# Performance work log

Measured on AMD Instinct MI355X. Metric: run time of the kernel, lower is better.

The kernel has to match this reference:

```python
import jax, jax.numpy as jnp
import numpy as np

HIDDEN = 1024
N_EXPERTS = 8
CAP_FACTOR = 1.1
LN_EPS = 1e-5


def setup_inputs() -> dict:
    key = jax.random.key(0)
    ks = jax.random.split(key, 8)
    d, E, dff = HIDDEN, N_EXPERTS, 4 * HIDDEN
    x = jax.random.normal(ks[0], (4, 2048, d), dtype=jnp.float32)
    gate_w = jax.random.normal(ks[1], (d, E), dtype=jnp.float32) / np.sqrt(d)
    ln_g = jnp.ones((E, d), dtype=jnp.float32)
    ln_b = jnp.zeros((E, d), dtype=jnp.float32)
    w1 = jax.random.normal(ks[2], (E, d, dff), dtype=jnp.float32) / np.sqrt(d)
    b1 = jnp.zeros((E, dff), dtype=jnp.float32)
    w2 = jax.random.normal(ks[3], (E, dff, d), dtype=jnp.float32) / np.sqrt(dff)
    b2 = jnp.zeros((E, d), dtype=jnp.float32)
    return {"x": x, "gate_w": gate_w, "ln_g": ln_g, "ln_b": ln_b,
            "w1": w1, "b1": b1, "w2": w2, "b2": b2}


def reference(x, gate_w, ln_g, ln_b, w1, b1, w2, b2):
    B, S, d = x.shape
    E = gate_w.shape[1]
    N = B * S
    cap = int(N / E * CAP_FACTOR)  # expert capacity

    xt = x.reshape(N, d)
    # Router: top-1 expert per token (max-subtract before softmax is a no-op)
    logits = xt @ gate_w                               # [N, E]
    probs = jax.nn.softmax(logits, axis=-1)
    eidx = jnp.argmax(probs, axis=-1)                  # [N] int

    onehot = jax.nn.one_hot(eidx, E, dtype=jnp.int32)  # [N, E]
    counts = onehot.sum(axis=0).astype(jnp.float32)    # pre-drop counts [E]

    # Deterministic capacity: keep first `cap` tokens per expert, drop rest.
    # (torch code drops randomly via multinomial; structure is identical.)
    pos = jnp.cumsum(onehot, axis=0) - 1               # [N, E]
    pos_tok = jnp.take_along_axis(pos, eidx[:, None], axis=1)[:, 0]  # [N]
    keep = (pos_tok < cap).astype(x.dtype)             # [N]
    pos_c = jnp.minimum(pos_tok, cap - 1)              # clamp; dropped tokens write zeros

    # Dispatch into per-expert buffers [E, cap, d]
    buf = jnp.zeros((E, cap, d), dtype=x.dtype).at[eidx, pos_c].add(xt * keep[:, None])

    # Per-expert FFN: LayerNorm -> Linear -> GELU -> Linear
    mu = buf.mean(axis=-1, keepdims=True)
    var = jnp.mean((buf - mu) ** 2, axis=-1, keepdims=True)
    nb = (buf - mu) * jax.lax.rsqrt(var + LN_EPS)
    nb = nb * ln_g[:, None, :] + ln_b[:, None, :]
    h = jax.nn.gelu(jnp.einsum('ecd,edf->ecf', nb, w1) + b1[:, None, :], approximate=False)
    y = jnp.einsum('ecf,efd->ecd', h, w2) + b2[:, None, :]  # [E, cap, d]

    # Combine: dropped tokens get zeros (matches torch output init)
    out_tok = y[eidx, pos_c] * keep[:, None]           # [N, d]
    output = out_tok.reshape(B, S, d)

    # Load-balancing loss: 1 - cosine(counts, uniform) * 0.01
    tokens_per_expert = N / E
    uniform = jnp.full((E,), tokens_per_expert, dtype=jnp.float32)
    cos = jnp.dot(counts, uniform) / (jnp.linalg.norm(counts) * jnp.linalg.norm(uniform) + 1e-8)
    loss = 1.0 - cos * 0.01
    return output, loss
```

## Files before the change

kernel.cpp:

```cpp
#include <hip/hip_runtime.h>
#include <cstdint>
#include <cstddef>

#define NTOK 8192
#define D    1024
#define DFF  4096
#define NEXP 8
#define CAP  1126
#define MPAD 1152

typedef float f32x4 __attribute__((ext_vector_type(4)));
typedef __bf16 bf16x8 __attribute__((ext_vector_type(8)));

__device__ inline unsigned short f2bf(float f) {
    unsigned u = __float_as_uint(f);
    u += 0x7fffu + ((u >> 16) & 1u);
    return (unsigned short)(u >> 16);
}

__device__ inline void gload16(const void* g, void* l) {
    __builtin_amdgcn_global_load_lds(
        (const __attribute__((address_space(1))) unsigned int*)g,
        (__attribute__((address_space(3))) unsigned int*)l,
        16, 0, 0);
}

__global__ __launch_bounds__(256) void router_kernel(
    const float* __restrict__ x, const float* __restrict__ gw, int* __restrict__ eidx)
{
    int tok  = blockIdx.x * 4 + (threadIdx.x >> 6);
    int lane = threadIdx.x & 63;
    const float* xr = x + (size_t)tok * D;
    float a[8] = {0.f,0.f,0.f,0.f,0.f,0.f,0.f,0.f};
    #pragma unroll
    for (int it = 0; it < D / 64; ++it) {
        int d = lane + it * 64;
        float xv = xr[d];
        const float4 g0 = *(const float4*)(gw + (size_t)d * 8);
        const float4 g1 = *(const float4*)(gw + (size_t)d * 8 + 4);
        a[0] += xv * g0.x; a[1] += xv * g0.y; a[2] += xv * g0.z; a[3] += xv * g0.w;
        a[4] += xv * g1.x; a[5] += xv * g1.y; a[6] += xv * g1.z; a[7] += xv * g1.w;
    }
    #pragma unroll
    for (int off = 32; off > 0; off >>= 1)
        #pragma unroll
        for (int e = 0; e < 8; ++e) a[e] += __shfl_xor(a[e], off, 64);
    if (lane == 0) {
        int bi = 0; float bv = a[0];
        #pragma unroll
        for (int e = 1; e < 8; ++e) if (a[e] > bv) { bv = a[e]; bi = e; }
        eidx[tok] = bi;
    }
}

__global__ __launch_bounds__(1024) void scan_kernel(
    const int* __restrict__ eidx, int* __restrict__ slot_map,
    int* __restrict__ kept_cnt, float* __restrict__ loss_out)
{
    __shared__ int sc[8][1024];
    int t = threadIdx.x;
    int le[8];
    int c[8] = {0,0,0,0,0,0,0,0};
    #pragma unroll
    for (int i = 0; i < 8; ++i) { le[i] = eidx[t * 8 + i]; c[le[i]]++; }
    int v[8];
    #pragma unroll
    for (int e = 0; e < 8; ++e) { v[e] = c[e]; sc[e][t] = v[e]; }
    __syncthreads();
    for (int s = 1; s < 1024; s <<= 1) {
        int add[8] = {0,0,0,0,0,0,0,0};
        if (t >= s) {
            #pragma unroll
            for (int e = 0; e < 8; ++e) add[e] = sc[e][t - s];
        }
        __syncthreads();
        #pragma unroll
        for (int e = 0; e < 8; ++e) { v[e] += add[e]; sc[e][t] = v[e]; }
        __syncthreads();
    }
    int base[8];
    #pragma unroll
    for (int e = 0; e < 8; ++e) base[e] = v[e] - c[e];
    #pragma unroll
    for (int i = 0; i < 8; ++i) {
        int e = le[i]; int pos = base[e]++;
        if (pos < CAP) slot_map[e * CAP + pos] = t * 8 + i;
    }
    if (t == 1023) {
        float dotv = 0.f, ss = 0.f;
        #pragma unroll
        for (int e = 0; e < 8; ++e) {
            float cf = (float)v[e];
            kept_cnt[e] = v[e] < CAP ? v[e] : CAP;
            dotv += cf * 1024.0f;
            ss   += cf * cf;
        }
        float denom = sqrtf(ss) * (1024.0f * sqrtf(8.0f)) + 1e-8f;
        loss_out[0] = 1.0f - 0.01f * (dotv / denom);
    }
}

__global__ __launch_bounds__(256) void zero_out(float4* __restrict__ p, int n)
{
    int stride = gridDim.x * blockDim.x;
    for (int i = blockIdx.x * blockDim.x + threadIdx.x; i < n; i += stride)
        p[i] = make_float4(0.f, 0.f, 0.f, 0.f);
}

__global__ __launch_bounds__(256) void dispatch_ln(
    const float* __restrict__ x, const float* __restrict__ lng, const float* __restrict__ lnb,
    const int* __restrict__ slot_map, const int* __restrict__ kept_cnt,
    unsigned short* __restrict__ xbuf)
{
    int p = blockIdx.x, e = blockIdx.y, tid = threadIdx.x;
    ushort4* dst = (ushort4*)(xbuf + ((size_t)e * MPAD + p) * D) + tid;
    if (p >= kept_cnt[e]) { *dst = make_ushort4(0, 0, 0, 0); return; }
    int tok = slot_map[e * CAP + p];
    const float4 xv = *((const float4*)(x + (size_t)tok * D) + tid);
    float s  = xv.x + xv.y + xv.z + xv.w;
    float ss = xv.x * xv.x + xv.y * xv.y + xv.z * xv.z + xv.w * xv.w;
    #pragma unroll
    for (int off = 32; off > 0; off >>= 1) {
        s  += __shfl_xor(s,  off, 64);
        ss += __shfl_xor(ss, off, 64);
    }
    __shared__ float red[8];
    int lane = tid & 63, wv = tid >> 6;
    if (lane == 0) { red[wv] = s; red[4 + wv] = ss; }
    __syncthreads();
    s  = red[0] + red[1] + red[2] + red[3];
    ss = red[4] + red[5] + red[6] + red[7];
    float mu = s * (1.0f / D);
    float rs = rsqrtf(ss * (1.0f / D) - mu * mu + 1e-5f);
    const float4 gv = *((const float4*)(lng + (size_t)e * D) + tid);
    const float4 bv = *((const float4*)(lnb + (size_t)e * D) + tid);
    ushort4 o;
    o.x = f2bf((xv.x - mu) * rs * gv.x + bv.x);
    o.y = f2bf((xv.y - mu) * rs * gv.y + bv.y);
    o.z = f2bf((xv.z - mu) * rs * gv.z + bv.z);
    o.w = f2bf((xv.w - mu) * rs * gv.w + bv.w);
    *dst = o;
}

__global__ __launch_bounds__(256) void transpose_bf16(
    const float* __restrict__ W, unsigned short* __restrict__ WT, int K, int N)
{
    __shared__ float t[64][65];
    int e = blockIdx.z;
    int n0 = blockIdx.x * 64, k0 = blockIdx.y * 64;
    const float* We = W + (size_t)e * K * N;
    unsigned short* WTe = WT + (size_t)e * K * N;
    int tx = threadIdx.x & 15, ty = threadIdx.x >> 4;
    #pragma unroll
    for (int j = 0; j < 4; ++j) {
        int k = ty + 16 * j;
        const float4 v = *(const float4*)(We + (size_t)(k0 + k) * N + n0 + tx * 4);
        t[k][tx * 4 + 0] = v.x; t[k][tx * 4 + 1] = v.y;
        t[k][tx * 4 + 2] = v.z; t[k][tx * 4 + 3] = v.w;
    }
    __syncthreads();
    #pragma unroll
    for (int j = 0; j < 4; ++j) {
        int n = ty + 16 * j;
        ushort4 o;
        o.x = f2bf(t[tx * 4 + 0][n]); o.y = f2bf(t[tx * 4 + 1][n]);
        o.z = f2bf(t[tx * 4 + 2][n]); o.w = f2bf(t[tx * 4 + 3][n]);
        *(ushort4*)(WTe + (size_t)(n0 + n) * K + k0 + tx * 4) = o;
    }
}

template<int K, int N, int MODE>
__global__ __launch_bounds__(256, 2) void gemm_kernel(
    const unsigned short* __restrict__ A,
    const unsigned short* __restrict__ BT,
    const float* __restrict__ bias,
    unsigned short* __restrict__ Hout,
    float* __restrict__ Yout,
    const int* __restrict__ slot_map,
    const int* __restrict__ kept_cnt)
{
    const int nb = blockIdx.x, mb = blockIdx.y, e = blockIdx.z;
    const int tid  = threadIdx.x;
    const int lane = tid & 63;
    const int l15  = lane & 15, lg = lane >> 4;
    const int wave = tid >> 6, wr = wave >> 1, wc = wave & 1;
    __shared__ __align__(16) char smem[16384];
    const unsigned short* Ae = A + ((size_t)e * MPAD + (size_t)mb * 128) * K;
    const unsigned short* Be = BT + ((size_t)e * N + (size_t)nb * 128) * K;
    f32x4 acc[4][4] = {};

    for (int kk = 0; kk < K / 32; ++kk) {
        __syncthreads();
        #pragma unroll
        for (int q = 0; q < 2; ++q) {
            int cid = q * 256 + tid;
            int row = cid >> 2, pp = cid & 3;
            int cc  = pp ^ ((row >> 1) & 3);
            gload16(Ae + (size_t)row * K + kk * 32 + cc * 8, smem + cid * 16);
            gload16(Be + (size_t)row * K + kk * 32 + cc * 8, smem + 8192 + cid * 16);
        }
        __syncthreads();
        bf16x8 af[4], bfr[4];
        #pragma unroll
        for (int i = 0; i < 4; ++i) {
            int ra = wr * 64 + i * 16 + l15;
            af[i]  = *(const bf16x8*)(smem + ra * 64 + ((lg ^ ((ra >> 1) & 3)) << 4));
            int rb = wc * 64 + i * 16 + l15;
            bfr[i] = *(const bf16x8*)(smem + 8192 + rb * 64 + ((lg ^ ((rb >> 1) & 3)) << 4));
        }
        #pragma unroll
        for (int mi = 0; mi < 4; ++mi)
            #pragma unroll
            for (int ni = 0; ni < 4; ++ni)
                acc[mi][ni] = __builtin_amdgcn_mfma_f32_16x16x32_bf16(
                    af[mi], bfr[ni], acc[mi][ni], 0, 0, 0);
    }

    const int kept = (MODE == 1) ? kept_cnt[e] : 0;
    #pragma unroll
    for (int mi = 0; mi < 4; ++mi) {
        #pragma unroll
        for (int ni = 0; ni < 4; ++ni) {
            int col = nb * 128 + wc * 64 + ni * 16 + l15;
            float bv = bias[(size_t)e * N + col];
            #pragma unroll
            for (int j = 0; j < 4; ++j) {
                int row = mb * 128 + wr * 64 + mi * 16 + 4 * lg + j;
                float v = acc[mi][ni][j] + bv;
                if (MODE == 0) {
                    v = 0.5f * v * (1.0f + erff(v * 0.70710678118654752f));
                    Hout[((size_t)e * MPAD + row) * N + col] = f2bf(v);
                } else {
                    if (row < kept) {
                        int tok = slot_map[e * CAP + row];
                        Yout[(size_t)tok * D + col] = v;
                    }
                }
            }
        }
    }
}

extern "C" void kernel_launch(void* const* d_in, const int* in_sizes, int n_in,
                              void* d_out, int out_size, void* d_ws, size_t ws_size,
                              hipStream_t stream)
{
    const float* x   = (const float*)d_in[0];
    const float* gw  = (const float*)d_in[1];
    const float* lng = (const float*)d_in[2];
    const float* lnb = (const float*)d_in[3];
    const float* w1  = (const float*)d_in[4];
    const float* b1  = (const float*)d_in[5];
    const float* w2  = (const float*)d_in[6];
    const float* b2  = (const float*)d_in[7];
    float* out = (float*)d_out;

    char* ws = (char*)d_ws;
    unsigned short* wT   = (unsigned short*)ws;
    unsigned short* xbuf = (unsigned short*)(ws + 67108864);
    unsigned short* hbuf = (unsigned short*)(ws + 67108864 + 18874368);
    int* eidx     = (int*)(ws + 161480704);
    int* slot_map = eidx + NTOK;
    int* kept     = slot_map + NEXP * CAP;

    router_kernel<<<NTOK / 4, 256, 0, stream>>>(x, gw, eidx);
    scan_kernel<<<1, 1024, 0, stream>>>(eidx, slot_map, kept, out + (size_t)NTOK * D);
    zero_out<<<2048, 256, 0, stream>>>((float4*)out, NTOK * D / 4);
    dispatch_ln<<<dim3(MPAD, NEXP), 256, 0, stream>>>(x, lng, lnb, slot_map, kept, xbuf);

    transpose_bf16<<<dim3(DFF / 64, D / 64, NEXP), 256, 0, stream>>>(w1, wT, D, DFF);
    gemm_kernel<D, DFF, 0><<<dim3(DFF / 128, MPAD / 128, NEXP), 256, 0, stream>>>(
        xbuf, wT, b1, hbuf, nullptr, slot_map, kept);

    transpose_bf16<<<dim3(D / 64, DFF / 64, NEXP), 256, 0, stream>>>(w2, wT, DFF, D);
    gemm_kernel<DFF, D, 1><<<dim3(D / 128, MPAD / 128, NEXP), 256, 0, stream>>>(
        hbuf, wT, b2, nullptr, out, slot_map, kept);
}
```

Measured before the change: 395.6 us.

## Double-buffer GEMM LDS tiles and swizzle block order across XCDs

The GEMM main loop now uses two LDS buffers, so the global-to-LDS load of the next K-slice is issued before the MFMA work on the current slice, which removes one barrier per iteration. The launch grid is flattened to 1D and remapped so that consecutive tiles sharing weight and activation panels land on the same XCD, which should improve L2 reuse. LDS per block doubles to 32 KB, which could lower occupancy, and the remap adds some integer arithmetic per block.

```diff
diff --git a/kernel.cpp b/kernel.cpp
--- a/kernel.cpp
+++ b/kernel.cpp
@@ -179,34 +179,49 @@
     const int* __restrict__ slot_map,
     const int* __restrict__ kept_cnt)
 {
-    const int nb = blockIdx.x, mb = blockIdx.y, e = blockIdx.z;
+    constexpr int MB = MPAD / 128;
+    constexpr int NB = N / 128;
+    const int T = NEXP * MB * NB;
+    const int orig = blockIdx.x;
+    const int q8 = T >> 3, r8 = T & 7;
+    const int xcd = orig & 7, ii = orig >> 3;
+    const int swz = (xcd < r8 ? xcd * (q8 + 1) : r8 * (q8 + 1) + (xcd - r8) * q8) + ii;
+    const int mb = swz % MB;
+    const int t2 = swz / MB;
+    const int nb = t2 % NB;
+    const int e  = t2 / NB;
+
     const int tid  = threadIdx.x;
     const int lane = tid & 63;
     const int l15  = lane & 15, lg = lane >> 4;
     const int wave = tid >> 6, wr = wave >> 1, wc = wave & 1;
-    __shared__ __align__(16) char smem[16384];
+    __shared__ __align__(16) char smem[32768];
     const unsigned short* Ae = A + ((size_t)e * MPAD + (size_t)mb * 128) * K;
     const unsigned short* Be = BT + ((size_t)e * N + (size_t)nb * 128) * K;
     f32x4 acc[4][4] = {};
 
-    for (int kk = 0; kk < K / 32; ++kk) {
-        __syncthreads();
+    auto stage = [&](int buf, int kk) {
+        char* sA = smem + buf * 16384;
+        char* sB = sA + 8192;
         #pragma unroll
         for (int q = 0; q < 2; ++q) {
             int cid = q * 256 + tid;
             int row = cid >> 2, pp = cid & 3;
             int cc  = pp ^ ((row >> 1) & 3);
-            gload16(Ae + (size_t)row * K + kk * 32 + cc * 8, smem + cid * 16);
-            gload16(Be + (size_t)row * K + kk * 32 + cc * 8, smem + 8192 + cid * 16);
-        }
-        __syncthreads();
+            gload16(Ae + (size_t)row * K + kk * 32 + cc * 8, sA + cid * 16);
+            gload16(Be + (size_t)row * K + kk * 32 + cc * 8, sB + cid * 16);
+        }
+    };
+    auto compute = [&](int buf) {
+        const char* sA = smem + buf * 16384;
+        const char* sB = sA + 8192;
         bf16x8 af[4], bfr[4];
         #pragma unroll
         for (int i = 0; i < 4; ++i) {
             int ra = wr * 64 + i * 16 + l15;
-            af[i]  = *(const bf16x8*)(smem + ra * 64 + ((lg ^ ((ra >> 1) & 3)) << 4));
+            af[i]  = *(const bf16x8*)(sA + ra * 64 + ((lg ^ ((ra >> 1) & 3)) << 4));
             int rb = wc * 64 + i * 16 + l15;
-            bfr[i] = *(const bf16x8*)(smem + 8192 + rb * 64 + ((lg ^ ((rb >> 1) & 3)) << 4));
+            bfr[i] = *(const bf16x8*)(sB + rb * 64 + ((lg ^ ((rb >> 1) & 3)) << 4));
         }
         #pragma unroll
         for (int mi = 0; mi < 4; ++mi)
@@ -214,7 +229,20 @@
             for (int ni = 0; ni < 4; ++ni)
                 acc[mi][ni] = __builtin_amdgcn_mfma_f32_16x16x32_bf16(
                     af[mi], bfr[ni], acc[mi][ni], 0, 0, 0);
-    }
+    };
+
+    stage(0, 0);
+    asm volatile("s_waitcnt vmcnt(0)" ::: "memory");
+    __syncthreads();
+    int cur = 0;
+    for (int kk = 0; kk + 1 < K / 32; ++kk) {
+        stage(cur ^ 1, kk + 1);
+        compute(cur);
+        asm volatile("s_waitcnt vmcnt(0)" ::: "memory");
+        __syncthreads();
+        cur ^= 1;
+    }
+    compute(cur);
 
     const int kept = (MODE == 1) ? kept_cnt[e] : 0;
     #pragma unroll
@@ -269,10 +297,10 @@
     dispatch_ln<<<dim3(MPAD, NEXP), 256, 0, stream>>>(x, lng, lnb, slot_map, kept, xbuf);
 
     transpose_bf16<<<dim3(DFF / 64, D / 64, NEXP), 256, 0, stream>>>(w1, wT, D, DFF);
-    gemm_kernel<D, DFF, 0><<<dim3(DFF / 128, MPAD / 128, NEXP), 256, 0, stream>>>(
+    gemm_kernel<D, DFF, 0><<<NEXP * (MPAD / 128) * (DFF / 128), 256, 0, stream>>>(
         xbuf, wT, b1, hbuf, nullptr, slot_map, kept);
 
     transpose_bf16<<<dim3(D / 64, DFF / 64, NEXP), 256, 0, stream>>>(w2, wT, DFF, D);
-    gemm_kernel<DFF, D, 1><<<dim3(D / 128, MPAD / 128, NEXP), 256, 0, stream>>>(
+    gemm_kernel<DFF, D, 1><<<NEXP * (MPAD / 128) * (D / 128), 256, 0, stream>>>(
         hbuf, wT, b2, nullptr, out, slot_map, kept);
 }
```

Result: faster. 336.1 us (-15.0%).
